# Kernel tuning notes

Measured on AMD Instinct MI355X. Metric: run time of the kernel, lower is better.

Reference implementation:

```python
import jax, jax.numpy as jnp
import numpy as np

N_NODES = 100000
N_EDGES = 1600000
NFEAT = 128
NHID = 128
NCLASS = 40
BN_EPS = 1e-5


def _glorot(key, shape):
    fan_in, fan_out = shape[1], shape[0]
    lim = (6.0 / (fan_in + fan_out)) ** 0.5
    return jax.random.uniform(key, shape, jnp.float32, -lim, lim)


def setup_inputs() -> dict:
    key = jax.random.key(0)
    ks = jax.random.split(key, 16)
    x = jax.random.normal(ks[0], (N_NODES, NFEAT), jnp.float32)
    src = jax.random.randint(ks[1], (N_EDGES,), 0, N_NODES, jnp.int64)
    dst = jax.random.randint(ks[2], (N_EDGES,), 0, N_NODES, jnp.int64)
    edge_index = jnp.stack([src, dst])  # [2, E]
    return {
        "x": x,
        "edge_index": edge_index,
        # conv1: nfeat -> nhid (lin_l with bias on aggregated msgs, lin_r no bias on root)
        "W1l": _glorot(ks[3], (NHID, NFEAT)), "b1": jnp.zeros((NHID,), jnp.float32),
        "W1r": _glorot(ks[4], (NHID, NFEAT)),
        # convx[0]: nhid -> nhid
        "Wxl": _glorot(ks[5], (NHID, NHID)), "bx": jnp.zeros((NHID,), jnp.float32),
        "Wxr": _glorot(ks[6], (NHID, NHID)),
        # conv2: nhid -> nclass
        "W2l": _glorot(ks[7], (NCLASS, NHID)), "b2": jnp.zeros((NCLASS,), jnp.float32),
        "W2r": _glorot(ks[8], (NCLASS, NHID)),
        # batch_norm3 (nhid) and batch_norm2 (nclass)
        "g3": jnp.ones((NHID,), jnp.float32), "be3": jnp.zeros((NHID,), jnp.float32),
        "g2": jnp.ones((NCLASS,), jnp.float32), "be2": jnp.zeros((NCLASS,), jnp.float32),
    }


def _sage_conv(x, src, dst, Wl, b, Wr):
    # mean aggregation of source features at destination nodes
    msg = x[src]                                                  # [E, F] gather
    agg = jax.ops.segment_sum(msg, dst, num_segments=N_NODES)    # [N, F] scatter-add
    cnt = jax.ops.segment_sum(jnp.ones((msg.shape[0],), x.dtype), dst, num_segments=N_NODES)
    mean = agg / jnp.maximum(cnt, 1.0)[:, None]                   # empty neighborhoods -> 0
    return mean @ Wl.T + b + x @ Wr.T


def _batch_norm(x, gamma, beta):
    mu = jnp.mean(x, axis=0)
    var = jnp.mean(jnp.square(x - mu), axis=0)  # biased var (training-mode BN)
    return (x - mu) * jax.lax.rsqrt(var + BN_EPS) * gamma + beta


def reference(x, edge_index, W1l, b1, W1r, Wxl, bx, Wxr, W2l, b2, W2r, g3, be3, g2, be2):
    src, dst = edge_index[0], edge_index[1]
    h = _sage_conv(x, src, dst, W1l, b1, W1r)      # conv1
    h = jax.nn.relu(h)
    # convx loop (nlayer - 2 == 1); dropout p=0 is identity
    h = _sage_conv(h, src, dst, Wxl, bx, Wxr)
    h = _batch_norm(h, g3, be3)                    # batch_norm3 (BN=True)
    h = jax.nn.relu(h)
    h = _sage_conv(h, src, dst, W2l, b2, W2r)      # conv2
    h = _batch_norm(h, g2, be2)                    # batch_norm2
    return h
```

## Files before the change

kernel.cpp:

```cpp
#include <hip/hip_runtime.h>
#include <hip/hip_bf16.h>

#define NN 100000
#define NE 1600000
#define NF 128
#define NC 40
#define BN_EPS 1e-5f

#define NB 256
#define NBU ((NN + 511) >> 9)
#define PT_TILE 4096
#define PT_GRID ((NE + PT_TILE - 1) / PT_TILE)
#define SBANK 32
#define NTILES (NN / 16)
#define LIN_GRID 1250
#define LIN80_GRID 512

typedef __attribute__((ext_vector_type(8))) short short8;
typedef __attribute__((ext_vector_type(4))) float float4v;
typedef __attribute__((ext_vector_type(4))) int int4v;

__device__ __forceinline__ unsigned short f2b(float f) {
    __hip_bfloat16 h = __float2bfloat16(f);
    return *reinterpret_cast<unsigned short*>(&h);
}
__device__ __forceinline__ float b2f_hi(unsigned u) { return __uint_as_float(u & 0xffff0000u); }
__device__ __forceinline__ float b2f_lo(unsigned u) { return __uint_as_float(u << 16); }


__global__ __launch_bounds__(256) void bhist_kernel(const int* __restrict__ dst,
                                                    int* __restrict__ bhist) {
    __shared__ int lh[NB];
    int tid = threadIdx.x;
    lh[tid] = 0;
    __syncthreads();
    int base = blockIdx.x * PT_TILE;
    int cnt = min(PT_TILE, NE - base);
    const int4v* d4 = (const int4v*)(dst + base);
    int cnt4 = cnt >> 2;
    for (int i = tid; i < cnt4; i += 256) {
        int4v d = __builtin_nontemporal_load(d4 + i);
        atomicAdd(&lh[d[0] >> 9], 1);
        atomicAdd(&lh[d[1] >> 9], 1);
        atomicAdd(&lh[d[2] >> 9], 1);
        atomicAdd(&lh[d[3] >> 9], 1);
    }
    __syncthreads();
    if (lh[tid]) atomicAdd(&bhist[tid], lh[tid]);
}

__global__ __launch_bounds__(256) void bscan_kernel(const int* __restrict__ bhist,
                                                    int* __restrict__ bbase,
                                                    int* __restrict__ bcur) {
    __shared__ int lds[NB];
    int t = threadIdx.x;
    int v = bhist[t];
    lds[t] = v;
    __syncthreads();
    for (int off = 1; off < NB; off <<= 1) {
        int u = (t >= off) ? lds[t - off] : 0;
        __syncthreads();
        lds[t] += u;
        __syncthreads();
    }
    int ex = lds[t] - v;
    bbase[t] = ex;
    bcur[t] = ex;
}

__global__ __launch_bounds__(256) void part_kernel(const int* __restrict__ src,
                                                   const int* __restrict__ dst,
                                                   int* __restrict__ bcur,
                                                   int2* __restrict__ stage) {
    __shared__ int2 pairs[PT_TILE];
    __shared__ int lhist[NB];
    __shared__ int gbase[NB];
    int tid = threadIdx.x;
    int base = blockIdx.x * PT_TILE;
    int cnt = min(PT_TILE, NE - base);
    int cnt4 = cnt >> 2;

    lhist[tid] = 0;
    __syncthreads();

    const int4v* d4 = (const int4v*)(dst + base);
    const int4v* s4 = (const int4v*)(src + base);
    for (int i = tid; i < cnt4; i += 256) {
        int4v d = __builtin_nontemporal_load(d4 + i);
        int4v s = __builtin_nontemporal_load(s4 + i);
#pragma unroll
        for (int j = 0; j < 4; ++j) {
            pairs[j * cnt4 + i] = make_int2(d[j], s[j]);
            atomicAdd(&lhist[d[j] >> 9], 1);
        }
    }
    __syncthreads();

    int c = lhist[tid];
    gbase[tid] = (c > 0) ? atomicAdd(&bcur[tid], c) : 0;
    lhist[tid] = 0;
    __syncthreads();

    for (int k = tid; k < cnt; k += 256) {
        int2 p = pairs[k];
        int b = p.x >> 9;
        int pos = atomicAdd(&lhist[b], 1);
        stage[gbase[b] + pos] = p;
    }
}

__global__ __launch_bounds__(256) void bucket_deg_kernel(const long long* __restrict__ stage,
                                                         const int* __restrict__ bbase,
                                                         const int* __restrict__ bcur,
                                                         int* __restrict__ deg) {
    int b = blockIdx.x;
    int s = bbase[b], e = bcur[b];
    for (int i = s + threadIdx.x; i < e; i += 256) {
        long long p = __builtin_nontemporal_load(stage + i);
        int d = (int)(p & 0xffffffffLL);
        atomicAdd(&deg[d], 1);
    }
}

__global__ __launch_bounds__(1024) void scan1_kernel(const int* __restrict__ deg,
                                                     int* __restrict__ row_loc,
                                                     int* __restrict__ blocksum) {
    __shared__ int lds[1024];
    int t = threadIdx.x;
    int i = blockIdx.x * 1024 + t;
    int v = (i < NN) ? deg[i] : 0;
    lds[t] = v;
    __syncthreads();
    for (int off = 1; off < 1024; off <<= 1) {
        int u = (t >= off) ? lds[t - off] : 0;
        __syncthreads();
        lds[t] += u;
        __syncthreads();
    }
    if (i < NN) row_loc[i] = lds[t] - v;
    if (t == 1023) blocksum[blockIdx.x] = lds[1023];
}

__global__ __launch_bounds__(128) void scan2_kernel(int* __restrict__ blocksum, int nb) {
    __shared__ int lds[128];
    int t = threadIdx.x;
    int v = (t < nb) ? blocksum[t] : 0;
    lds[t] = v;
    __syncthreads();
    for (int off = 1; off < 128; off <<= 1) {
        int u = (t >= off) ? lds[t - off] : 0;
        __syncthreads();
        lds[t] += u;
        __syncthreads();
    }
    if (t < nb) blocksum[t] = lds[t] - v;
}

__global__ __launch_bounds__(1024) void scan3_kernel(const int* __restrict__ deg,
                                                     const int* __restrict__ row_loc,
                                                     const int* __restrict__ blockoff,
                                                     int* __restrict__ row_ptr,
                                                     float* __restrict__ inv_cnt) {
    int i = blockIdx.x * 1024 + threadIdx.x;
    if (i < NN) {
        row_ptr[i] = blockoff[blockIdx.x] + row_loc[i];
        int d = deg[i];
        inv_cnt[i] = 1.0f / (float)(d > 0 ? d : 1);
    }
    if (i == 0) row_ptr[NN] = NE;
}

__global__ __launch_bounds__(256) void bucket_fill_kernel(const long long* __restrict__ stage,
                                                          const int* __restrict__ bbase,
                                                          const int* __restrict__ bcur,
                                                          const int* __restrict__ row_ptr,
                                                          int* __restrict__ cursor,
                                                          int* __restrict__ csr) {
    int b = blockIdx.x;
    int s = bbase[b], e = bcur[b];
    for (int i = s + threadIdx.x; i < e; i += 256) {
        long long p = __builtin_nontemporal_load(stage + i);
        int d = (int)(p & 0xffffffffLL);
        int sv = (int)(p >> 32);
        int pos = atomicAdd(&cursor[d], 1);
        csr[row_ptr[d] + pos] = sv;
    }
}


__global__ __launch_bounds__(256) void f2b4_kernel(const float* __restrict__ in,
                                                   unsigned short* __restrict__ out, int n4) {
    int i = blockIdx.x * 256 + threadIdx.x;
    if (i < n4) {
        float4 v = ((const float4*)in)[i];
        ushort4 o;
        o.x = f2b(v.x); o.y = f2b(v.y); o.z = f2b(v.z); o.w = f2b(v.w);
        ((ushort4*)out)[i] = o;
    }
}


__global__ __launch_bounds__(64) void pack_w_kernel(const float* __restrict__ Wl,
                                                    const float* __restrict__ Wr,
                                                    unsigned short* __restrict__ Bp) {
    int nt = blockIdx.x & 7;
    int kk = blockIdx.x >> 3;
    int lane = threadIdx.x;
    int n = nt * 16 + (lane & 15);
    int kb = kk * 32 + (lane >> 4) * 8;
    size_t base = ((size_t)(kk * 8 + nt) * 64 + lane) * 8;
#pragma unroll
    for (int j = 0; j < 8; ++j) {
        int k = kb + j;
        float v = (k < NF) ? Wl[(size_t)n * NF + k] : Wr[(size_t)n * NF + (k - NF)];
        Bp[base + j] = f2b(v);
    }
}

__global__ __launch_bounds__(64) void pack_w80_kernel(const float* __restrict__ Wl,
                                                      const float* __restrict__ Wr,
                                                      unsigned short* __restrict__ Bp) {
    int nt = blockIdx.x % 5;
    int kk = blockIdx.x / 5;
    int lane = threadIdx.x;
    int n = nt * 16 + (lane & 15);
    int kb = kk * 32 + (lane >> 4) * 8;
    size_t base = ((size_t)(kk * 5 + nt) * 64 + lane) * 8;
#pragma unroll
    for (int j = 0; j < 8; ++j) {
        int k = kb + j;
        float v = (n < NC) ? Wl[(size_t)n * NF + k] : Wr[(size_t)(n - NC) * NF + k];
        Bp[base + j] = f2b(v);
    }
}


__device__ __forceinline__ void acc8(float* a, uint4 u) {
    a[0] += b2f_lo(u.x); a[1] += b2f_hi(u.x);
    a[2] += b2f_lo(u.y); a[3] += b2f_hi(u.y);
    a[4] += b2f_lo(u.z); a[5] += b2f_hi(u.z);
    a[6] += b2f_lo(u.w); a[7] += b2f_hi(u.w);
}

__global__ __launch_bounds__(256) void agg_mean_bf16(const unsigned short* __restrict__ X,
                                                     const int* __restrict__ csr,
                                                     const int* __restrict__ row_ptr,
                                                     const float* __restrict__ inv_cnt,
                                                     unsigned short* __restrict__ out) {
    int tid = threadIdx.x;
    int lane = tid & 63;
    int wave = tid >> 6;
    int qw = lane >> 4;
    int sl = lane & 15;
    int n = blockIdx.x * 16 + wave * 4 + qw;
    if (n >= NN) return;
    int s = row_ptr[n], e = row_ptr[n + 1];
    int foff = sl * 8;

    float a[8];
#pragma unroll
    for (int j = 0; j < 8; ++j) a[j] = 0.f;

    int i = s;
    for (; i + 4 <= e; i += 4) {
        int s0 = csr[i], s1 = csr[i + 1], s2 = csr[i + 2], s3 = csr[i + 3];
        uint4 u0 = *(const uint4*)(X + (size_t)s0 * NF + foff);
        uint4 u1 = *(const uint4*)(X + (size_t)s1 * NF + foff);
        uint4 u2 = *(const uint4*)(X + (size_t)s2 * NF + foff);
        uint4 u3 = *(const uint4*)(X + (size_t)s3 * NF + foff);
        acc8(a, u0); acc8(a, u1); acc8(a, u2); acc8(a, u3);
    }
    for (; i < e; ++i) {
        uint4 u = *(const uint4*)(X + (size_t)csr[i] * NF + foff);
        acc8(a, u);
    }

    float ic = inv_cnt[n];
    uint4 o;
    o.x = (unsigned)f2b(a[0] * ic) | ((unsigned)f2b(a[1] * ic) << 16);
    o.y = (unsigned)f2b(a[2] * ic) | ((unsigned)f2b(a[3] * ic) << 16);
    o.z = (unsigned)f2b(a[4] * ic) | ((unsigned)f2b(a[5] * ic) << 16);
    o.w = (unsigned)f2b(a[6] * ic) | ((unsigned)f2b(a[7] * ic) << 16);
    *(uint4*)(out + (size_t)n * NF + foff) = o;
}


template <bool RELU, bool STATS>
__device__ __forceinline__ void lin_body(const unsigned short* __restrict__ Ab,
                                         const unsigned short* __restrict__ Xb,
                                         const unsigned short* __restrict__ Bp,
                                         const float* __restrict__ bias,
                                         unsigned short* __restrict__ outb,
                                         float* __restrict__ sums,
                                         float* ls) {
    __shared__ short8 Bs[4096];
    int tid = threadIdx.x;
    int wave = tid >> 6;
    int lane = tid & 63;
    int quad = lane >> 4;
    int sl = lane & 15;
    const short8* Bv = (const short8*)Bp;

    if (STATS) ls[tid] = 0.f;
#pragma unroll
    for (int c = 0; c < 16; ++c) Bs[c * 256 + tid] = Bv[c * 256 + tid];
    __syncthreads();

    float4v bias4[2];
#pragma unroll
    for (int j = 0; j < 2; ++j)
        bias4[j] = *(const float4v*)(bias + (2 * wave + j) * 16 + quad * 4);

    float sts[2][4], stq[2][4];
    if (STATS) {
#pragma unroll
        for (int j = 0; j < 2; ++j)
#pragma unroll
            for (int r = 0; r < 4; ++r) { sts[j][r] = 0.f; stq[j][r] = 0.f; }
    }

    for (int t = blockIdx.x; t < NTILES; t += LIN_GRID) {
        int rr = t * 16 + sl;
        const unsigned short* arow = Ab + (size_t)rr * NF;
        const unsigned short* xrow = Xb + (size_t)rr * NF;

        short8 xf[8];
#pragma unroll
        for (int kk = 0; kk < 8; ++kk) {
            int kb = (kk & 3) * 32 + quad * 8;
            const unsigned short* asrc = (kk < 4) ? arow : xrow;
            xf[kk] = *(const short8*)(asrc + kb);
        }

        float4v acc[2];
#pragma unroll
        for (int j = 0; j < 2; ++j) acc[j] = (float4v){0.f, 0.f, 0.f, 0.f};

#pragma unroll
        for (int kk = 0; kk < 8; ++kk) {
            short8 b0 = Bs[(kk * 8 + 2 * wave + 0) * 64 + lane];
            short8 b1 = Bs[(kk * 8 + 2 * wave + 1) * 64 + lane];
            acc[0] = __builtin_amdgcn_mfma_f32_16x16x32_bf16(b0, xf[kk], acc[0], 0, 0, 0);
            acc[1] = __builtin_amdgcn_mfma_f32_16x16x32_bf16(b1, xf[kk], acc[1], 0, 0, 0);
        }

#pragma unroll
        for (int j = 0; j < 2; ++j) {
            int c0 = (2 * wave + j) * 16 + quad * 4;
            float v0 = acc[j][0] + bias4[j][0];
            float v1 = acc[j][1] + bias4[j][1];
            float v2 = acc[j][2] + bias4[j][2];
            float v3 = acc[j][3] + bias4[j][3];
            if (RELU) {
                v0 = fmaxf(v0, 0.f); v1 = fmaxf(v1, 0.f);
                v2 = fmaxf(v2, 0.f); v3 = fmaxf(v3, 0.f);
            }
            if (STATS) {
                sts[j][0] += v0; stq[j][0] += v0 * v0;
                sts[j][1] += v1; stq[j][1] += v1 * v1;
                sts[j][2] += v2; stq[j][2] += v2 * v2;
                sts[j][3] += v3; stq[j][3] += v3 * v3;
            }
            ushort4 o;
            o.x = f2b(v0); o.y = f2b(v1); o.z = f2b(v2); o.w = f2b(v3);
            *(ushort4*)(outb + (size_t)rr * NF + c0) = o;
        }
    }

    if (STATS) {
#pragma unroll
        for (int j = 0; j < 2; ++j) {
            int c0 = (2 * wave + j) * 16 + quad * 4;
#pragma unroll
            for (int r = 0; r < 4; ++r) {
                atomicAdd(&ls[c0 + r], sts[j][r]);
                atomicAdd(&ls[128 + c0 + r], stq[j][r]);
            }
        }
        __syncthreads();
        atomicAdd(&sums[(blockIdx.x & (SBANK - 1)) * 256 + tid], ls[tid]);
    }
}

__global__ __launch_bounds__(256, 2) void lin_conv1_kernel(const unsigned short* __restrict__ Ab,
                                                           const unsigned short* __restrict__ Xb,
                                                           const unsigned short* __restrict__ Bp,
                                                           const float* __restrict__ bias,
                                                           unsigned short* __restrict__ outb) {
    lin_body<true, false>(Ab, Xb, Bp, bias, outb, nullptr, nullptr);
}

__global__ __launch_bounds__(256, 2) void lin_convx_kernel(const unsigned short* __restrict__ Ab,
                                                           const unsigned short* __restrict__ Xb,
                                                           const unsigned short* __restrict__ Bp,
                                                           const float* __restrict__ bias,
                                                           unsigned short* __restrict__ outb,
                                                           float* __restrict__ sums) {
    __shared__ float ls[256];
    lin_body<false, true>(Ab, Xb, Bp, bias, outb, sums, ls);
}


__global__ __launch_bounds__(128) void bn3_coef_kernel(const float* __restrict__ sums,
                                                       const float* __restrict__ g,
                                                       const float* __restrict__ be,
                                                       float* __restrict__ sc,
                                                       float* __restrict__ sh) {
    int c = threadIdx.x;
    float sv = 0.f, qv = 0.f;
    for (int b = 0; b < SBANK; ++b) {
        sv += sums[b * 256 + c];
        qv += sums[b * 256 + 128 + c];
    }
    float invN = 1.0f / (float)NN;
    float mu = sv * invN;
    float var = qv * invN - mu * mu;
    float s = rsqrtf(var + BN_EPS) * g[c];
    sc[c] = s;
    sh[c] = be[c] - mu * s;
}


__global__ __launch_bounds__(256, 2) void lin80_mfma_kernel(const unsigned short* __restrict__ Xb,
                                                            const unsigned short* __restrict__ Bp,
                                                            const float* __restrict__ b2,
                                                            const float* __restrict__ bnsc,
                                                            const float* __restrict__ bnsh,
                                                            unsigned short* __restrict__ t40,
                                                            float* __restrict__ z40) {
    __shared__ short8 Bs[1280];
    __shared__ float scs[128], shs[128];
    int tid = threadIdx.x;
    int wave = tid >> 6;
    int lane = tid & 63;
    int quad = lane >> 4;
    int sl = lane & 15;
    const short8* Bv = (const short8*)Bp;

    for (int c = tid; c < 1280; c += 256) Bs[c] = Bv[c];
    if (tid < 128) { scs[tid] = bnsc[tid]; shs[tid] = bnsh[tid]; }
    __syncthreads();

    int gw = blockIdx.x * 4 + wave;
    for (int t = gw; t < NTILES; t += LIN80_GRID * 4) {
        int rr = t * 16 + sl;
        const unsigned short* xrow = Xb + (size_t)rr * NF;

        float4v acc[5];
#pragma unroll
        for (int nt = 0; nt < 5; ++nt) acc[nt] = (float4v){0.f, 0.f, 0.f, 0.f};

#pragma unroll
        for (int kk = 0; kk < 4; ++kk) {
            int kb = kk * 32 + quad * 8;
            uint4 u = *(const uint4*)(xrow + kb);
            float4v c0 = *(const float4v*)(scs + kb);
            float4v c1 = *(const float4v*)(scs + kb + 4);
            float4v h0 = *(const float4v*)(shs + kb);
            float4v h1 = *(const float4v*)(shs + kb + 4);
            short8 xf;
            xf[0] = (short)f2b(fmaxf(b2f_lo(u.x) * c0[0] + h0[0], 0.f));
            xf[1] = (short)f2b(fmaxf(b2f_hi(u.x) * c0[1] + h0[1], 0.f));
            xf[2] = (short)f2b(fmaxf(b2f_lo(u.y) * c0[2] + h0[2], 0.f));
            xf[3] = (short)f2b(fmaxf(b2f_hi(u.y) * c0[3] + h0[3], 0.f));
            xf[4] = (short)f2b(fmaxf(b2f_lo(u.z) * c1[0] + h1[0], 0.f));
            xf[5] = (short)f2b(fmaxf(b2f_hi(u.z) * c1[1] + h1[1], 0.f));
            xf[6] = (short)f2b(fmaxf(b2f_lo(u.w) * c1[2] + h1[2], 0.f));
            xf[7] = (short)f2b(fmaxf(b2f_hi(u.w) * c1[3] + h1[3], 0.f));
#pragma unroll
            for (int nt = 0; nt < 5; ++nt) {
                short8 bfr = Bs[(kk * 5 + nt) * 64 + lane];
                acc[nt] = __builtin_amdgcn_mfma_f32_16x16x32_bf16(bfr, xf, acc[nt], 0, 0, 0);
            }
        }

#pragma unroll
        for (int nt = 0; nt < 5; ++nt) {
            int c0 = nt * 16 + quad * 4;
            if (c0 < NC) {
                ushort4 o;
                o.x = f2b(acc[nt][0]); o.y = f2b(acc[nt][1]);
                o.z = f2b(acc[nt][2]); o.w = f2b(acc[nt][3]);
                *(ushort4*)(t40 + (size_t)rr * NC + c0) = o;
            } else {
                float4 bz = *(const float4*)(b2 + c0 - NC);
                float4 o;
                o.x = acc[nt][0] + bz.x; o.y = acc[nt][1] + bz.y;
                o.z = acc[nt][2] + bz.z; o.w = acc[nt][3] + bz.w;
                *(float4*)(z40 + (size_t)rr * NC + (c0 - NC)) = o;
            }
        }
    }
}


__global__ __launch_bounds__(256) void agg40_add_bf16(const unsigned short* __restrict__ T,
                                                      const float* __restrict__ Z,
                                                      const int* __restrict__ csr,
                                                      const int* __restrict__ row_ptr,
                                                      const float* __restrict__ inv_cnt,
                                                      float* __restrict__ out) {
    int tid = threadIdx.x;
    int lane = tid & 63;
    int wave = tid >> 6;
    if (lane >= 60) return;
    int sub = lane / 20;
    int sl = lane % 20;
    int n = blockIdx.x * 12 + wave * 3 + sub;
    if (n >= NN) return;
    int s = row_ptr[n], e = row_ptr[n + 1];
    const unsigned short* Tf = T + sl * 2;
    float a0 = 0.f, a1 = 0.f;
    int i = s;
    for (; i + 4 <= e; i += 4) {
        int s0 = csr[i], s1 = csr[i + 1], s2 = csr[i + 2], s3 = csr[i + 3];
        unsigned u0 = *(const unsigned*)(Tf + (size_t)s0 * NC);
        unsigned u1 = *(const unsigned*)(Tf + (size_t)s1 * NC);
        unsigned u2 = *(const unsigned*)(Tf + (size_t)s2 * NC);
        unsigned u3 = *(const unsigned*)(Tf + (size_t)s3 * NC);
        a0 += b2f_lo(u0) + b2f_lo(u1) + b2f_lo(u2) + b2f_lo(u3);
        a1 += b2f_hi(u0) + b2f_hi(u1) + b2f_hi(u2) + b2f_hi(u3);
    }
    for (; i < e; ++i) {
        unsigned u = *(const unsigned*)(Tf + (size_t)csr[i] * NC);
        a0 += b2f_lo(u);
        a1 += b2f_hi(u);
    }
    float ic = inv_cnt[n];
    const float2 zv = *(const float2*)(Z + (size_t)n * NC + sl * 2);
    float2 o;
    o.x = a0 * ic + zv.x;
    o.y = a1 * ic + zv.y;
    *(float2*)(out + (size_t)n * NC + sl * 2) = o;
}

#define BN_GRID 640

template <int F>
__global__ __launch_bounds__(256) void bn_stats2_kernel(const float* __restrict__ X,
                                                        float* __restrict__ sums) {
    __shared__ float ls[2 * F];
    int tid = threadIdx.x;
    for (int i = tid; i < 2 * F; i += 256) ls[i] = 0.f;
    __syncthreads();

    const int total4 = NN * F / 4;
    const int stride = BN_GRID * 256;
    int i0 = blockIdx.x * 256 + tid;
    int c0 = (i0 * 4) % F;
    float s0 = 0.f, s1 = 0.f, s2 = 0.f, s3 = 0.f;
    float q0 = 0.f, q1 = 0.f, q2 = 0.f, q3 = 0.f;
    for (int i = i0; i < total4; i += stride) {
        float4 v = ((const float4*)X)[i];
        s0 += v.x; q0 += v.x * v.x;
        s1 += v.y; q1 += v.y * v.y;
        s2 += v.z; q2 += v.z * v.z;
        s3 += v.w; q3 += v.w * v.w;
    }
    atomicAdd(&ls[c0 + 0], s0); atomicAdd(&ls[F + c0 + 0], q0);
    atomicAdd(&ls[c0 + 1], s1); atomicAdd(&ls[F + c0 + 1], q1);
    atomicAdd(&ls[c0 + 2], s2); atomicAdd(&ls[F + c0 + 2], q2);
    atomicAdd(&ls[c0 + 3], s3); atomicAdd(&ls[F + c0 + 3], q3);
    __syncthreads();
    for (int i = tid; i < 2 * F; i += 256) atomicAdd(&sums[i], ls[i]);
}

template <bool RELU>
__global__ __launch_bounds__(256) void bn_apply_kernel(float* __restrict__ X,
                                                       const float* __restrict__ sums,
                                                       const float* __restrict__ g,
                                                       const float* __restrict__ be,
                                                       int F, float invN) {
    size_t idx = (size_t)blockIdx.x * blockDim.x + threadIdx.x;
    size_t total = (size_t)NN * F;
    if (idx >= total) return;
    int t = (int)(idx % F);
    float mu = sums[t] * invN;
    float var = sums[F + t] * invN - mu * mu;
    float scale = rsqrtf(var + BN_EPS) * g[t];
    float v = (X[idx] - mu) * scale + be[t];
    if (RELU) v = fmaxf(v, 0.f);
    X[idx] = v;
}


extern "C" void kernel_launch(void* const* d_in, const int* in_sizes, int n_in,
                              void* d_out, int out_size, void* d_ws, size_t ws_size,
                              hipStream_t stream) {
    const float* x   = (const float*)d_in[0];
    const int*   ei  = (const int*)d_in[1];
    const int*   srcv = ei;
    const int*   dstv = ei + NE;
    const float* W1l = (const float*)d_in[2];
    const float* b1  = (const float*)d_in[3];
    const float* W1r = (const float*)d_in[4];
    const float* Wxl = (const float*)d_in[5];
    const float* bx  = (const float*)d_in[6];
    const float* Wxr = (const float*)d_in[7];
    const float* W2l = (const float*)d_in[8];
    const float* b2  = (const float*)d_in[9];
    const float* W2r = (const float*)d_in[10];
    const float* g3  = (const float*)d_in[11];
    const float* be3 = (const float*)d_in[12];
    const float* g2  = (const float*)d_in[13];
    const float* be2 = (const float*)d_in[14];
    float* out = (float*)d_out;

    char* w = (char*)d_ws;
    unsigned short* xb   = (unsigned short*)w; w += (size_t)NN * NF * 2;
    unsigned short* h1b  = (unsigned short*)w; w += (size_t)NN * NF * 2;
    unsigned short* aggb = (unsigned short*)w; w += (size_t)NN * NF * 2;
    unsigned short* h2b  = (unsigned short*)w; w += (size_t)NN * NF * 2;
    int* csr     = (int*)w; w += (size_t)NE * 4;
    int* row_ptr = (int*)w; w += (size_t)(NN + 4) * 4;
    int* deg     = (int*)w; w += (size_t)NN * 4;
    int* cursor  = (int*)w; w += (size_t)NN * 4;
    int* row_loc = (int*)w; w += (size_t)NN * 4;
    int* blocksum = (int*)w; w += 128 * 4;
    float* inv_cnt = (float*)w; w += (size_t)NN * 4;
    float* bnbuf3  = (float*)w; w += (size_t)SBANK * 256 * 4;
    float* bnbuf2  = (float*)w; w += 2 * NC * 4;
    float* bnsc    = (float*)w; w += NF * 4;
    float* bnsh    = (float*)w; w += NF * 4;
    unsigned short* Bp1 = (unsigned short*)w; w += (size_t)256 * NF * 2;
    unsigned short* Bpx = (unsigned short*)w; w += (size_t)256 * NF * 2;
    unsigned short* Bp2 = (unsigned short*)w; w += (size_t)128 * 80 * 2;
    int* bhist = (int*)w; w += NB * 4;
    int* bbase = (int*)w; w += NB * 4;
    int* bcurA = (int*)w; w += NB * 4;
    int2* stage = (int2*)h2b;
    unsigned short* t40 = xb;
    float* z40 = (float*)h1b;

    const int nscan = (NN + 1023) / 1024;

    hipMemsetAsync(deg, 0, (size_t)NN * 4, stream);
    hipMemsetAsync(cursor, 0, (size_t)NN * 4, stream);
    hipMemsetAsync(bhist, 0, NB * 4, stream);
    hipMemsetAsync(bnbuf3, 0, (size_t)SBANK * 256 * 4, stream);
    hipMemsetAsync(bnbuf2, 0, 2 * NC * 4, stream);

    bhist_kernel<<<PT_GRID, 256, 0, stream>>>(dstv, bhist);
    bscan_kernel<<<1, 256, 0, stream>>>(bhist, bbase, bcurA);
    part_kernel<<<PT_GRID, 256, 0, stream>>>(srcv, dstv, bcurA, stage);
    bucket_deg_kernel<<<NBU, 256, 0, stream>>>((const long long*)stage, bbase, bcurA, deg);
    scan1_kernel<<<nscan, 1024, 0, stream>>>(deg, row_loc, blocksum);
    scan2_kernel<<<1, 128, 0, stream>>>(blocksum, nscan);
    scan3_kernel<<<nscan, 1024, 0, stream>>>(deg, row_loc, blocksum, row_ptr, inv_cnt);
    bucket_fill_kernel<<<NBU, 256, 0, stream>>>((const long long*)stage, bbase, bcurA,
                                                row_ptr, cursor, csr);

    f2b4_kernel<<<(NN * NF / 4 + 255) / 256, 256, 0, stream>>>(x, xb, NN * NF / 4);
    pack_w_kernel<<<64, 64, 0, stream>>>(W1l, W1r, Bp1);
    pack_w_kernel<<<64, 64, 0, stream>>>(Wxl, Wxr, Bpx);
    pack_w80_kernel<<<20, 64, 0, stream>>>(W2l, W2r, Bp2);

    const int nblk_agg = (NN + 15) / 16;

    agg_mean_bf16<<<nblk_agg, 256, 0, stream>>>(xb, csr, row_ptr, inv_cnt, aggb);
    lin_conv1_kernel<<<LIN_GRID, 256, 0, stream>>>(aggb, xb, Bp1, b1, h1b);

    agg_mean_bf16<<<nblk_agg, 256, 0, stream>>>(h1b, csr, row_ptr, inv_cnt, aggb);
    lin_convx_kernel<<<LIN_GRID, 256, 0, stream>>>(aggb, h1b, Bpx, bx, h2b, bnbuf3);

    bn3_coef_kernel<<<1, 128, 0, stream>>>(bnbuf3, g3, be3, bnsc, bnsh);

    lin80_mfma_kernel<<<LIN80_GRID, 256, 0, stream>>>(h2b, Bp2, b2, bnsc, bnsh, t40, z40);
    agg40_add_bf16<<<(NN + 11) / 12, 256, 0, stream>>>(t40, z40, csr, row_ptr, inv_cnt, out);

    bn_stats2_kernel<NC><<<BN_GRID, 256, 0, stream>>>(out, bnbuf2);
    bn_apply_kernel<false><<<(NN * NC + 255) / 256, 256, 0, stream>>>(out, bnbuf2, g2, be2, NC, 1.0f / NN);
}
```

Before: 564.6 us.

## Fuse mean aggregation with MFMA linear layer per 16-node tile

Each of the first two SAGE convolutions now runs as one kernel. A block gathers and averages neighbour rows for 16 nodes, stages the mean and root rows in shared memory, and applies the packed weight matrix with MFMA in place. This drops the aggregated intermediate buffer's write and re-read, and one launch per layer. In exchange, each block reloads the full weight fragments from global memory into registers rather than from a persistent shared-memory copy, and BN statistics move to per-element shared atomics spread over more banks.

```diff
diff --git a/kernel.cpp b/kernel.cpp
--- a/kernel.cpp
+++ b/kernel.cpp
@@ -11,9 +11,8 @@
 #define NBU ((NN + 511) >> 9)
 #define PT_TILE 4096
 #define PT_GRID ((NE + PT_TILE - 1) / PT_TILE)
-#define SBANK 32
+#define SBANK2 256
 #define NTILES (NN / 16)
-#define LIN_GRID 1250
 #define LIN80_GRID 512
 
 typedef __attribute__((ext_vector_type(8))) short short8;
@@ -235,44 +234,63 @@
 }
 
 
-__device__ __forceinline__ void acc8(float* a, uint4 u) {
-    a[0] += b2f_lo(u.x); a[1] += b2f_hi(u.x);
-    a[2] += b2f_lo(u.y); a[3] += b2f_hi(u.y);
-    a[4] += b2f_lo(u.z); a[5] += b2f_hi(u.z);
-    a[6] += b2f_lo(u.w); a[7] += b2f_hi(u.w);
-}
-
-__global__ __launch_bounds__(256) void agg_mean_bf16(const unsigned short* __restrict__ X,
-                                                     const int* __restrict__ csr,
-                                                     const int* __restrict__ row_ptr,
-                                                     const float* __restrict__ inv_cnt,
-                                                     unsigned short* __restrict__ out) {
+#define LROW 136
+
+template <bool RELU, bool STATS>
+__device__ __forceinline__ void fused_conv_body(const unsigned short* __restrict__ X,
+                                                const int* __restrict__ csr,
+                                                const int* __restrict__ row_ptr,
+                                                const float* __restrict__ inv_cnt,
+                                                const unsigned short* __restrict__ Bp,
+                                                const float* __restrict__ bias,
+                                                unsigned short* __restrict__ outb,
+                                                float* __restrict__ sums,
+                                                float* ls) {
+    __shared__ unsigned short Ar[16 * LROW];
+    __shared__ unsigned short Xr[16 * LROW];
     int tid = threadIdx.x;
     int lane = tid & 63;
     int wave = tid >> 6;
     int qw = lane >> 4;
     int sl = lane & 15;
-    int n = blockIdx.x * 16 + wave * 4 + qw;
-    if (n >= NN) return;
+    int quad = qw;
+    int node = wave * 4 + qw;
+    int n = blockIdx.x * 16 + node;
+    int foff = sl * 8;
+
+    if (STATS) ls[tid] = 0.f;
+
+    uint4 ux = *(const uint4*)(X + (size_t)n * NF + foff);
+
     int s = row_ptr[n], e = row_ptr[n + 1];
-    int foff = sl * 8;
-
     float a[8];
 #pragma unroll
     for (int j = 0; j < 8; ++j) a[j] = 0.f;
 
-    int i = s;
-    for (; i + 4 <= e; i += 4) {
-        int s0 = csr[i], s1 = csr[i + 1], s2 = csr[i + 2], s3 = csr[i + 3];
-        uint4 u0 = *(const uint4*)(X + (size_t)s0 * NF + foff);
-        uint4 u1 = *(const uint4*)(X + (size_t)s1 * NF + foff);
-        uint4 u2 = *(const uint4*)(X + (size_t)s2 * NF + foff);
-        uint4 u3 = *(const uint4*)(X + (size_t)s3 * NF + foff);
-        acc8(a, u0); acc8(a, u1); acc8(a, u2); acc8(a, u3);
-    }
-    for (; i < e; ++i) {
-        uint4 u = *(const uint4*)(X + (size_t)csr[i] * NF + foff);
-        acc8(a, u);
+    {
+        int i = s;
+        for (; i + 4 <= e; i += 4) {
+            int s0 = csr[i], s1 = csr[i + 1], s2 = csr[i + 2], s3 = csr[i + 3];
+            uint4 u0 = *(const uint4*)(X + (size_t)s0 * NF + foff);
+            uint4 u1 = *(const uint4*)(X + (size_t)s1 * NF + foff);
+            uint4 u2 = *(const uint4*)(X + (size_t)s2 * NF + foff);
+            uint4 u3 = *(const uint4*)(X + (size_t)s3 * NF + foff);
+            a[0] += b2f_lo(u0.x) + b2f_lo(u1.x) + b2f_lo(u2.x) + b2f_lo(u3.x);
+            a[1] += b2f_hi(u0.x) + b2f_hi(u1.x) + b2f_hi(u2.x) + b2f_hi(u3.x);
+            a[2] += b2f_lo(u0.y) + b2f_lo(u1.y) + b2f_lo(u2.y) + b2f_lo(u3.y);
+            a[3] += b2f_hi(u0.y) + b2f_hi(u1.y) + b2f_hi(u2.y) + b2f_hi(u3.y);
+            a[4] += b2f_lo(u0.z) + b2f_lo(u1.z) + b2f_lo(u2.z) + b2f_lo(u3.z);
+            a[5] += b2f_hi(u0.z) + b2f_hi(u1.z) + b2f_hi(u2.z) + b2f_hi(u3.z);
+            a[6] += b2f_lo(u0.w) + b2f_lo(u1.w) + b2f_lo(u2.w) + b2f_lo(u3.w);
+            a[7] += b2f_hi(u0.w) + b2f_hi(u1.w) + b2f_hi(u2.w) + b2f_hi(u3.w);
+        }
+        for (; i < e; ++i) {
+            uint4 u = *(const uint4*)(X + (size_t)csr[i] * NF + foff);
+            a[0] += b2f_lo(u.x); a[1] += b2f_hi(u.x);
+            a[2] += b2f_lo(u.y); a[3] += b2f_hi(u.y);
+            a[4] += b2f_lo(u.z); a[5] += b2f_hi(u.z);
+            a[6] += b2f_lo(u.w); a[7] += b2f_hi(u.w);
+        }
     }
 
     float ic = inv_cnt[n];
@@ -281,123 +299,89 @@
     o.y = (unsigned)f2b(a[2] * ic) | ((unsigned)f2b(a[3] * ic) << 16);
     o.z = (unsigned)f2b(a[4] * ic) | ((unsigned)f2b(a[5] * ic) << 16);
     o.w = (unsigned)f2b(a[6] * ic) | ((unsigned)f2b(a[7] * ic) << 16);
-    *(uint4*)(out + (size_t)n * NF + foff) = o;
-}
-
-
-template <bool RELU, bool STATS>
-__device__ __forceinline__ void lin_body(const unsigned short* __restrict__ Ab,
-                                         const unsigned short* __restrict__ Xb,
-                                         const unsigned short* __restrict__ Bp,
-                                         const float* __restrict__ bias,
-                                         unsigned short* __restrict__ outb,
-                                         float* __restrict__ sums,
-                                         float* ls) {
-    __shared__ short8 Bs[4096];
-    int tid = threadIdx.x;
-    int wave = tid >> 6;
-    int lane = tid & 63;
-    int quad = lane >> 4;
-    int sl = lane & 15;
+    *(uint4*)(Ar + node * LROW + foff) = o;
+    *(uint4*)(Xr + node * LROW + foff) = ux;
+    __syncthreads();
+
     const short8* Bv = (const short8*)Bp;
-
-    if (STATS) ls[tid] = 0.f;
-#pragma unroll
-    for (int c = 0; c < 16; ++c) Bs[c * 256 + tid] = Bv[c * 256 + tid];
-    __syncthreads();
+    short8 bfr[8][2];
+#pragma unroll
+    for (int kk = 0; kk < 8; ++kk)
+#pragma unroll
+        for (int j = 0; j < 2; ++j)
+            bfr[kk][j] = Bv[(kk * 8 + 2 * wave + j) * 64 + lane];
+
+    short8 xf[8];
+#pragma unroll
+    for (int kk = 0; kk < 8; ++kk) {
+        int kb = (kk & 3) * 32 + quad * 8;
+        const unsigned short* src = (kk < 4 ? Ar : Xr) + sl * LROW + kb;
+        xf[kk] = *(const short8*)src;
+    }
 
     float4v bias4[2];
 #pragma unroll
     for (int j = 0; j < 2; ++j)
         bias4[j] = *(const float4v*)(bias + (2 * wave + j) * 16 + quad * 4);
 
-    float sts[2][4], stq[2][4];
+    float4v acc[2];
+#pragma unroll
+    for (int j = 0; j < 2; ++j) acc[j] = (float4v){0.f, 0.f, 0.f, 0.f};
+#pragma unroll
+    for (int kk = 0; kk < 8; ++kk) {
+        acc[0] = __builtin_amdgcn_mfma_f32_16x16x32_bf16(bfr[kk][0], xf[kk], acc[0], 0, 0, 0);
+        acc[1] = __builtin_amdgcn_mfma_f32_16x16x32_bf16(bfr[kk][1], xf[kk], acc[1], 0, 0, 0);
+    }
+
+    int rr = blockIdx.x * 16 + sl;
+#pragma unroll
+    for (int j = 0; j < 2; ++j) {
+        int c0 = (2 * wave + j) * 16 + quad * 4;
+        float v0 = acc[j][0] + bias4[j][0];
+        float v1 = acc[j][1] + bias4[j][1];
+        float v2 = acc[j][2] + bias4[j][2];
+        float v3 = acc[j][3] + bias4[j][3];
+        if (RELU) {
+            v0 = fmaxf(v0, 0.f); v1 = fmaxf(v1, 0.f);
+            v2 = fmaxf(v2, 0.f); v3 = fmaxf(v3, 0.f);
+        }
+        if (STATS) {
+            atomicAdd(&ls[c0 + 0], v0); atomicAdd(&ls[128 + c0 + 0], v0 * v0);
+            atomicAdd(&ls[c0 + 1], v1); atomicAdd(&ls[128 + c0 + 1], v1 * v1);
+            atomicAdd(&ls[c0 + 2], v2); atomicAdd(&ls[128 + c0 + 2], v2 * v2);
+            atomicAdd(&ls[c0 + 3], v3); atomicAdd(&ls[128 + c0 + 3], v3 * v3);
+        }
+        ushort4 ov;
+        ov.x = f2b(v0); ov.y = f2b(v1); ov.z = f2b(v2); ov.w = f2b(v3);
+        *(ushort4*)(outb + (size_t)rr * NF + c0) = ov;
+    }
+
     if (STATS) {
-#pragma unroll
-        for (int j = 0; j < 2; ++j)
-#pragma unroll
-            for (int r = 0; r < 4; ++r) { sts[j][r] = 0.f; stq[j][r] = 0.f; }
-    }
-
-    for (int t = blockIdx.x; t < NTILES; t += LIN_GRID) {
-        int rr = t * 16 + sl;
-        const unsigned short* arow = Ab + (size_t)rr * NF;
-        const unsigned short* xrow = Xb + (size_t)rr * NF;
-
-        short8 xf[8];
-#pragma unroll
-        for (int kk = 0; kk < 8; ++kk) {
-            int kb = (kk & 3) * 32 + quad * 8;
-            const unsigned short* asrc = (kk < 4) ? arow : xrow;
-            xf[kk] = *(const short8*)(asrc + kb);
-        }
-
-        float4v acc[2];
-#pragma unroll
-        for (int j = 0; j < 2; ++j) acc[j] = (float4v){0.f, 0.f, 0.f, 0.f};
-
-#pragma unroll
-        for (int kk = 0; kk < 8; ++kk) {
-            short8 b0 = Bs[(kk * 8 + 2 * wave + 0) * 64 + lane];
-            short8 b1 = Bs[(kk * 8 + 2 * wave + 1) * 64 + lane];
-            acc[0] = __builtin_amdgcn_mfma_f32_16x16x32_bf16(b0, xf[kk], acc[0], 0, 0, 0);
-            acc[1] = __builtin_amdgcn_mfma_f32_16x16x32_bf16(b1, xf[kk], acc[1], 0, 0, 0);
-        }
-
-#pragma unroll
-        for (int j = 0; j < 2; ++j) {
-            int c0 = (2 * wave + j) * 16 + quad * 4;
-            float v0 = acc[j][0] + bias4[j][0];
-            float v1 = acc[j][1] + bias4[j][1];
-            float v2 = acc[j][2] + bias4[j][2];
-            float v3 = acc[j][3] + bias4[j][3];
-            if (RELU) {
-                v0 = fmaxf(v0, 0.f); v1 = fmaxf(v1, 0.f);
-                v2 = fmaxf(v2, 0.f); v3 = fmaxf(v3, 0.f);
-            }
-            if (STATS) {
-                sts[j][0] += v0; stq[j][0] += v0 * v0;
-                sts[j][1] += v1; stq[j][1] += v1 * v1;
-                sts[j][2] += v2; stq[j][2] += v2 * v2;
-                sts[j][3] += v3; stq[j][3] += v3 * v3;
-            }
-            ushort4 o;
-            o.x = f2b(v0); o.y = f2b(v1); o.z = f2b(v2); o.w = f2b(v3);
-            *(ushort4*)(outb + (size_t)rr * NF + c0) = o;
-        }
-    }
-
-    if (STATS) {
-#pragma unroll
-        for (int j = 0; j < 2; ++j) {
-            int c0 = (2 * wave + j) * 16 + quad * 4;
-#pragma unroll
-            for (int r = 0; r < 4; ++r) {
-                atomicAdd(&ls[c0 + r], sts[j][r]);
-                atomicAdd(&ls[128 + c0 + r], stq[j][r]);
-            }
-        }
         __syncthreads();
-        atomicAdd(&sums[(blockIdx.x & (SBANK - 1)) * 256 + tid], ls[tid]);
-    }
-}
-
-__global__ __launch_bounds__(256, 2) void lin_conv1_kernel(const unsigned short* __restrict__ Ab,
-                                                           const unsigned short* __restrict__ Xb,
-                                                           const unsigned short* __restrict__ Bp,
-                                                           const float* __restrict__ bias,
-                                                           unsigned short* __restrict__ outb) {
-    lin_body<true, false>(Ab, Xb, Bp, bias, outb, nullptr, nullptr);
-}
-
-__global__ __launch_bounds__(256, 2) void lin_convx_kernel(const unsigned short* __restrict__ Ab,
-                                                           const unsigned short* __restrict__ Xb,
-                                                           const unsigned short* __restrict__ Bp,
-                                                           const float* __restrict__ bias,
-                                                           unsigned short* __restrict__ outb,
-                                                           float* __restrict__ sums) {
+        atomicAdd(&sums[(blockIdx.x & (SBANK2 - 1)) * 256 + tid], ls[tid]);
+    }
+}
+
+__global__ __launch_bounds__(256) void fused_conv1_kernel(const unsigned short* __restrict__ X,
+                                                          const int* __restrict__ csr,
+                                                          const int* __restrict__ row_ptr,
+                                                          const float* __restrict__ inv_cnt,
+                                                          const unsigned short* __restrict__ Bp,
+                                                          const float* __restrict__ bias,
+                                                          unsigned short* __restrict__ outb) {
+    fused_conv_body<true, false>(X, csr, row_ptr, inv_cnt, Bp, bias, outb, nullptr, nullptr);
+}
+
+__global__ __launch_bounds__(256) void fused_convx_kernel(const unsigned short* __restrict__ X,
+                                                          const int* __restrict__ csr,
+                                                          const int* __restrict__ row_ptr,
+                                                          const float* __restrict__ inv_cnt,
+                                                          const unsigned short* __restrict__ Bp,
+                                                          const float* __restrict__ bias,
+                                                          unsigned short* __restrict__ outb,
+                                                          float* __restrict__ sums) {
     __shared__ float ls[256];
-    lin_body<false, true>(Ab, Xb, Bp, bias, outb, sums, ls);
+    fused_conv_body<false, true>(X, csr, row_ptr, inv_cnt, Bp, bias, outb, sums, ls);
 }
 
 
@@ -408,7 +392,7 @@
                                                        float* __restrict__ sh) {
     int c = threadIdx.x;
     float sv = 0.f, qv = 0.f;
-    for (int b = 0; b < SBANK; ++b) {
+    for (int b = 0; b < SBANK2; ++b) {
         sv += sums[b * 256 + c];
         qv += sums[b * 256 + 128 + c];
     }
@@ -609,7 +593,6 @@
     char* w = (char*)d_ws;
     unsigned short* xb   = (unsigned short*)w; w += (size_t)NN * NF * 2;
     unsigned short* h1b  = (unsigned short*)w; w += (size_t)NN * NF * 2;
-    unsigned short* aggb = (unsigned short*)w; w += (size_t)NN * NF * 2;
     unsigned short* h2b  = (unsigned short*)w; w += (size_t)NN * NF * 2;
     int* csr     = (int*)w; w += (size_t)NE * 4;
     int* row_ptr = (int*)w; w += (size_t)(NN + 4) * 4;
@@ -618,7 +601,7 @@
     int* row_loc = (int*)w; w += (size_t)NN * 4;
     int* blocksum = (int*)w; w += 128 * 4;
     float* inv_cnt = (float*)w; w += (size_t)NN * 4;
-    float* bnbuf3  = (float*)w; w += (size_t)SBANK * 256 * 4;
+    float* bnbuf3  = (float*)w; w += (size_t)SBANK2 * 256 * 4;
     float* bnbuf2  = (float*)w; w += 2 * NC * 4;
     float* bnsc    = (float*)w; w += NF * 4;
     float* bnsh    = (float*)w; w += NF * 4;
@@ -637,7 +620,7 @@
     hipMemsetAsync(deg, 0, (size_t)NN * 4, stream);
     hipMemsetAsync(cursor, 0, (size_t)NN * 4, stream);
     hipMemsetAsync(bhist, 0, NB * 4, stream);
-    hipMemsetAsync(bnbuf3, 0, (size_t)SBANK * 256 * 4, stream);
+    hipMemsetAsync(bnbuf3, 0, (size_t)SBANK2 * 256 * 4, stream);
     hipMemsetAsync(bnbuf2, 0, 2 * NC * 4, stream);
 
     bhist_kernel<<<PT_GRID, 256, 0, stream>>>(dstv, bhist);
@@ -655,13 +638,9 @@
     pack_w_kernel<<<64, 64, 0, stream>>>(Wxl, Wxr, Bpx);
     pack_w80_kernel<<<20, 64, 0, stream>>>(W2l, W2r, Bp2);
 
-    const int nblk_agg = (NN + 15) / 16;
-
-    agg_mean_bf16<<<nblk_agg, 256, 0, stream>>>(xb, csr, row_ptr, inv_cnt, aggb);
-    lin_conv1_kernel<<<LIN_GRID, 256, 0, stream>>>(aggb, xb, Bp1, b1, h1b);
-
-    agg_mean_bf16<<<nblk_agg, 256, 0, stream>>>(h1b, csr, row_ptr, inv_cnt, aggb);
-    lin_convx_kernel<<<LIN_GRID, 256, 0, stream>>>(aggb, h1b, Bpx, bx, h2b, bnbuf3);
+    fused_conv1_kernel<<<NTILES, 256, 0, stream>>>(xb, csr, row_ptr, inv_cnt, Bp1, b1, h1b);
+
+    fused_convx_kernel<<<NTILES, 256, 0, stream>>>(h1b, csr, row_ptr, inv_cnt, Bpx, bx, h2b, bnbuf3);
 
     bn3_coef_kernel<<<1, 128, 0, stream>>>(bnbuf3, g3, be3, bnsc, bnsh);
 
```

Measured after the change: 626.0 us. +10.9%, slower.
